# Kernel optimization log

Hardware: AMD Instinct MI355X
Metric: run time of the kernel (lower is better)

Reference implementation:

```python
import jax, jax.numpy as jnp
import numpy as np

N, E, D, H = 100000, 800000, 64, 8
DV = D // H  # v_layer output dim


def setup_inputs() -> dict:
    key = jax.random.key(0)
    ks = jax.random.split(key, 16)
    s = lambda fan_in: 1.0 / np.sqrt(fan_in)
    return {
        "atom_feat": jax.random.normal(ks[0], (N, D), jnp.float32),
        "bond_feat": jax.random.normal(ks[1], (E, D), jnp.float32),
        "edge_idx": jax.random.randint(ks[2], (E, 2), 0, N, jnp.int32),
        # v_layer: input_dim -> input_dim // att_heads
        "Wv": jax.random.normal(ks[3], (D, DV), jnp.float32) * s(D),
        "bv": jnp.zeros((DV,), jnp.float32),
        # final_att: Linear(3D, D) -> ReLU -> Linear(D, D) -> ReLU -> Linear(D, H)
        "W1": jax.random.normal(ks[4], (3 * D, D), jnp.float32) * s(3 * D),
        "b1": jnp.zeros((D,), jnp.float32),
        "W2": jax.random.normal(ks[5], (D, D), jnp.float32) * s(D),
        "b2": jnp.zeros((D,), jnp.float32),
        "W3": jax.random.normal(ks[6], (D, H), jnp.float32) * s(D),
        "b3": jnp.zeros((H,), jnp.float32),
        # conv_layer: D -> D
        "Wc": jax.random.normal(ks[7], (D, D), jnp.float32) * s(D),
        "bc": jnp.zeros((D,), jnp.float32),
        # bond_layer: 2D -> D
        "Wb": jax.random.normal(ks[8], (2 * D, D), jnp.float32) * s(2 * D),
        "bb": jnp.zeros((D,), jnp.float32),
    }


def reference(atom_feat, bond_feat, edge_idx, Wv, bv, W1, b1, W2, b2, W3, b3, Wc, bc, Wb, bb):
    n = atom_feat.shape[0]
    src, dst = edge_idx[:, 0], edge_idx[:, 1]

    # edge attention MLP: [E, 3D] -> [E, H]
    x_att = jnp.concatenate([atom_feat[dst], atom_feat[src], bond_feat], axis=-1)
    h = jax.nn.relu(x_att @ W1 + b1)
    h = jax.nn.relu(h @ W2 + b2)
    logits = h @ W3 + b3  # [E, H]

    # scatter-softmax over edges grouped by src
    seg_max = jax.ops.segment_max(logits, src, num_segments=n)
    e = jnp.exp(logits - seg_max[src])
    denom = jax.ops.segment_sum(e, src, num_segments=n)
    att = e / denom[src]  # [E, H]

    # attention-weighted scatter-sum of values
    v = atom_feat @ Wv + bv  # [N, DV]
    msg = att[:, None, :] * v[dst][:, :, None]  # [E, DV, H]
    agg = jax.ops.segment_sum(msg, src, num_segments=n)  # [N, DV, H]

    out = agg.reshape(n, -1) @ Wc + bc  # [N, D]

    # bond update
    nb = jnp.concatenate([out[dst] + out[src], bond_feat], axis=-1)  # [E, 2D]
    new_bond_feat = jax.nn.relu(nb @ Wb + bb)

    # residual + activation
    out = jax.nn.relu(atom_feat + out)
    return out, new_bond_feat
```

## Files before the change

### kernel.cpp

```cpp
#include <hip/hip_runtime.h>
#include <math.h>

#define NA 100000
#define NE 800000

typedef __attribute__((ext_vector_type(8))) short short8;
typedef __attribute__((ext_vector_type(4))) float f32x4;

__device__ __forceinline__ unsigned fmap(float f) {
    unsigned b = __float_as_uint(f);
    return (b & 0x80000000u) ? ~b : (b | 0x80000000u);
}
__device__ __forceinline__ float funmap(unsigned u) {
    unsigned b = (u & 0x80000000u) ? (u ^ 0x80000000u) : ~u;
    return __uint_as_float(b);
}
__device__ __forceinline__ unsigned short f2bf(float f) {
    unsigned u = __float_as_uint(f);
    u += 0x7fffu + ((u >> 16) & 1u);
    return (unsigned short)(u >> 16);
}

__device__ __forceinline__ short8 ldsfrag(const unsigned short* p) {
    return *(const short8*)p;
}

__global__ void k_v(const float* __restrict__ af, const float* __restrict__ Wv,
                    const float* __restrict__ bv, float* __restrict__ v) {
    __shared__ float sWv[512];
    __shared__ float sbv[8];
    int t = threadIdx.x;
    for (int i = t; i < 512; i += 256) sWv[i] = Wv[i];
    if (t < 8) sbv[t] = bv[t];
    __syncthreads();
    int gid = blockIdx.x * 256 + t;
    if (gid >= NA * 8) return;
    int n = gid >> 3, i = gid & 7;
    const float* ar = af + (long)n * 64;
    float acc = sbv[i];
#pragma unroll
    for (int k = 0; k < 64; k++) acc += ar[k] * sWv[k * 8 + i];
    v[gid] = acc;
}

__global__ __launch_bounds__(256) void k_edge_mlp(
    const float* __restrict__ af, const float* __restrict__ bond,
    const int* __restrict__ eidx,
    const float* __restrict__ W1, const float* __restrict__ b1,
    const float* __restrict__ W2, const float* __restrict__ b2,
    const float* __restrict__ W3, const float* __restrict__ b3,
    float* __restrict__ logits, unsigned* __restrict__ segmax) {
    __shared__ unsigned short sW1T[4][24][16][8];
    __shared__ unsigned short sW2T[4][8][16][8];
    __shared__ unsigned short sW3T[8][16][8];
    __shared__ unsigned short sX[4][24][16][8];
    __shared__ int sED[4][16][2];

    int tid = threadIdx.x;
    for (int idx = tid; idx < 192 * 64; idx += 256) {
        int k = idx >> 6, n = idx & 63;
        sW1T[n >> 4][k >> 3][n & 15][k & 7] = f2bf(W1[idx]);
    }
    for (int idx = tid; idx < 64 * 64; idx += 256) {
        int k = idx >> 6, n = idx & 63;
        sW2T[n >> 4][k >> 3][n & 15][k & 7] = f2bf(W2[idx]);
    }
    for (int idx = tid; idx < 8 * 16 * 8; idx += 256) ((unsigned short*)sW3T)[idx] = 0;
    __syncthreads();
    for (int idx = tid; idx < 64 * 8; idx += 256) {
        int k = idx >> 3, o = idx & 7;
        sW3T[k >> 3][o][k & 7] = f2bf(W3[idx]);
    }
    __syncthreads();

    int lane = tid & 63, wv = tid >> 6;
    int l15 = lane & 15, lq = lane >> 4;
    float b1v[4], b2v[4];
#pragma unroll
    for (int t = 0; t < 4; t++) { b1v[t] = b1[t * 16 + l15]; b2v[t] = b2[t * 16 + l15]; }
    float b3v = (l15 < 8) ? b3[l15] : 0.f;

    long stride = (long)gridDim.x * 64;
    for (long base = ((long)blockIdx.x * 4 + wv) * 16; base < NE; base += stride) {
        if (lane < 16) {
            int2 sd = ((const int2*)eidx)[base + lane];
            sED[wv][lane][0] = sd.x;
            sED[wv][lane][1] = sd.y;
        }
#pragma unroll
        for (int it = 0; it < 12; it++) {
            int q = it * 64 + lane;
            int e = q / 48;
            int r = q - e * 48;
            const float* sp;
            if (r < 16)      sp = af + (long)sED[wv][e][1] * 64 + r * 4;
            else if (r < 32) sp = af + (long)sED[wv][e][0] * 64 + (r - 16) * 4;
            else             sp = bond + (base + e) * 64 + (long)(r - 32) * 4;
            float4 xv = *(const float4*)sp;
            ushort4 p;
            p.x = f2bf(xv.x); p.y = f2bf(xv.y); p.z = f2bf(xv.z); p.w = f2bf(xv.w);
            *(ushort4*)&sX[wv][r >> 1][e][(r & 1) * 4] = p;
        }

        f32x4 acc[4] = {{0,0,0,0},{0,0,0,0},{0,0,0,0},{0,0,0,0}};
#pragma unroll
        for (int ks = 0; ks < 6; ks++) {
            short8 a = ldsfrag(&sX[wv][ks * 4 + lq][l15][0]);
#pragma unroll
            for (int t = 0; t < 4; t++) {
                short8 b = ldsfrag(&sW1T[t][ks * 4 + lq][l15][0]);
                acc[t] = __builtin_amdgcn_mfma_f32_16x16x32_bf16(a, b, acc[t], 0, 0, 0);
            }
        }
#pragma unroll
        for (int t = 0; t < 4; t++)
#pragma unroll
            for (int r = 0; r < 4; r++) {
                float h = fmaxf(acc[t][r] + b1v[t], 0.f);
                sX[wv][2 * t + ((lane >> 3) & 1)][lq * 4 + r][lane & 7] = f2bf(h);
            }

        f32x4 acc2[4] = {{0,0,0,0},{0,0,0,0},{0,0,0,0},{0,0,0,0}};
#pragma unroll
        for (int ks = 0; ks < 2; ks++) {
            short8 a = ldsfrag(&sX[wv][ks * 4 + lq][l15][0]);
#pragma unroll
            for (int t = 0; t < 4; t++) {
                short8 b = ldsfrag(&sW2T[t][ks * 4 + lq][l15][0]);
                acc2[t] = __builtin_amdgcn_mfma_f32_16x16x32_bf16(a, b, acc2[t], 0, 0, 0);
            }
        }
#pragma unroll
        for (int t = 0; t < 4; t++)
#pragma unroll
            for (int r = 0; r < 4; r++) {
                float h = fmaxf(acc2[t][r] + b2v[t], 0.f);
                sX[wv][2 * t + ((lane >> 3) & 1)][lq * 4 + r][lane & 7] = f2bf(h);
            }

        f32x4 accL = {0, 0, 0, 0};
#pragma unroll
        for (int ks = 0; ks < 2; ks++) {
            short8 a = ldsfrag(&sX[wv][ks * 4 + lq][l15][0]);
            short8 b = ldsfrag(&sW3T[ks * 4 + lq][l15][0]);
            accL = __builtin_amdgcn_mfma_f32_16x16x32_bf16(a, b, accL, 0, 0, 0);
        }
        if (l15 < 8) {
#pragma unroll
            for (int r = 0; r < 4; r++) {
                int m = lq * 4 + r;
                float lg = accL[r] + b3v;
                long e = base + m;
                logits[e * 8 + l15] = lg;
                atomicMax(&segmax[(long)sED[wv][m][0] * 8 + l15], fmap(lg));
            }
        }
    }
}

__global__ void k_exp_denom(const int* __restrict__ eidx,
                            const float* __restrict__ logits,
                            const unsigned* __restrict__ segmax,
                            float* __restrict__ denom) {
    long gid = (long)blockIdx.x * 256 + threadIdx.x;
    if (gid >= (long)NE * 8) return;
    long e = gid >> 3;
    int o = gid & 7;
    int src = eidx[2 * e];
    float m = funmap(segmax[(long)src * 8 + o]);
    float ex = __expf(logits[gid] - m);
    atomicAdd(&denom[(long)src * 8 + o], ex);
}

__global__ void k_agg(const int* __restrict__ eidx,
                      const float* __restrict__ logits,
                      const unsigned* __restrict__ segmax,
                      const float* __restrict__ denom,
                      const float* __restrict__ v,
                      float* __restrict__ agg) {
    int t = threadIdx.x;
    int lane = t & 63, wv = t >> 6;
    long e = (long)blockIdx.x * 4 + wv;
    if (e >= NE) return;
    int2 sd = ((const int2*)eidx)[e];
    int src = sd.x, dst = sd.y;
    int o = lane & 7;
    int i = lane >> 3;
    float lg = logits[e * 8 + o];
    float m = funmap(segmax[(long)src * 8 + o]);
    float den = denom[(long)src * 8 + o];
    float att = __expf(lg - m) / den;
    float val = att * v[(long)dst * 8 + i];
    atomicAdd(&agg[(long)src * 64 + lane], val);
}

__global__ __launch_bounds__(256) void k_out(
    const float* __restrict__ agg, const float* __restrict__ Wc,
    const float* __restrict__ bc, const float* __restrict__ af,
    float* __restrict__ out_pre, float* __restrict__ out_final) {
    __shared__ float sWc[64 * 64];
    int t = threadIdx.x;
    for (int i = t; i < 4096; i += 256) sWc[i] = Wc[i];
    __syncthreads();
    int lane = t & 63, wv = t >> 6;
    float bcv = bc[lane];
    long stride = (long)gridDim.x * 4;
    for (long n = (long)blockIdx.x * 4 + wv; n < NA; n += stride) {
        float a = agg[n * 64 + lane];
        float acc = bcv;
#pragma unroll 4
        for (int k = 0; k < 64; k++) acc += __shfl(a, k) * sWc[k * 64 + lane];
        out_pre[n * 64 + lane] = acc;
        out_final[n * 64 + lane] = fmaxf(af[n * 64 + lane] + acc, 0.f);
    }
}

__global__ __launch_bounds__(256) void k_bond_out(
    const float* __restrict__ out_pre, const float* __restrict__ bond,
    const int* __restrict__ eidx, const float* __restrict__ Wb,
    const float* __restrict__ bb, float* __restrict__ nbf) {
    __shared__ unsigned short sWbT[4][16][16][8];
    __shared__ unsigned short sXB[4][16][16][8];
    __shared__ int sEDB[4][16][2];

    int tid = threadIdx.x;
    for (int idx = tid; idx < 128 * 64; idx += 256) {
        int k = idx >> 6, n = idx & 63;
        sWbT[n >> 4][k >> 3][n & 15][k & 7] = f2bf(Wb[idx]);
    }
    __syncthreads();

    int lane = tid & 63, wv = tid >> 6;
    int l15 = lane & 15, lq = lane >> 4;
    float bbv[4];
#pragma unroll
    for (int t = 0; t < 4; t++) bbv[t] = bb[t * 16 + l15];

    long stride = (long)gridDim.x * 64;
    for (long base = ((long)blockIdx.x * 4 + wv) * 16; base < NE; base += stride) {
        if (lane < 16) {
            int2 sd = ((const int2*)eidx)[base + lane];
            sEDB[wv][lane][0] = sd.x;
            sEDB[wv][lane][1] = sd.y;
        }
#pragma unroll
        for (int it = 0; it < 8; it++) {
            int q = it * 64 + lane;
            int e = q >> 5;
            int r = q & 31;
            float4 xv;
            if (r < 16) {
                const float4* pa = (const float4*)(out_pre + (long)sEDB[wv][e][1] * 64 + r * 4);
                const float4* pb = (const float4*)(out_pre + (long)sEDB[wv][e][0] * 64 + r * 4);
                float4 a = *pa, b = *pb;
                xv.x = a.x + b.x; xv.y = a.y + b.y; xv.z = a.z + b.z; xv.w = a.w + b.w;
            } else {
                xv = *(const float4*)(bond + (base + e) * 64 + (long)(r - 16) * 4);
            }
            ushort4 p;
            p.x = f2bf(xv.x); p.y = f2bf(xv.y); p.z = f2bf(xv.z); p.w = f2bf(xv.w);
            *(ushort4*)&sXB[wv][r >> 1][e][(r & 1) * 4] = p;
        }

        f32x4 acc[4] = {{0,0,0,0},{0,0,0,0},{0,0,0,0},{0,0,0,0}};
#pragma unroll
        for (int ks = 0; ks < 4; ks++) {
            short8 a = ldsfrag(&sXB[wv][ks * 4 + lq][l15][0]);
#pragma unroll
            for (int t = 0; t < 4; t++) {
                short8 b = ldsfrag(&sWbT[t][ks * 4 + lq][l15][0]);
                acc[t] = __builtin_amdgcn_mfma_f32_16x16x32_bf16(a, b, acc[t], 0, 0, 0);
            }
        }
#pragma unroll
        for (int t = 0; t < 4; t++)
#pragma unroll
            for (int r = 0; r < 4; r++) {
                long m = base + lq * 4 + r;
                nbf[m * 64 + t * 16 + l15] = fmaxf(acc[t][r] + bbv[t], 0.f);
            }
    }
}

extern "C" void kernel_launch(void* const* d_in, const int* in_sizes, int n_in,
                              void* d_out, int out_size, void* d_ws, size_t ws_size,
                              hipStream_t stream) {
    const float* af   = (const float*)d_in[0];
    const float* bond = (const float*)d_in[1];
    const int*   eidx = (const int*)d_in[2];
    const float* Wv = (const float*)d_in[3];
    const float* bv = (const float*)d_in[4];
    const float* W1 = (const float*)d_in[5];
    const float* b1 = (const float*)d_in[6];
    const float* W2 = (const float*)d_in[7];
    const float* b2 = (const float*)d_in[8];
    const float* W3 = (const float*)d_in[9];
    const float* b3 = (const float*)d_in[10];
    const float* Wc = (const float*)d_in[11];
    const float* bc = (const float*)d_in[12];
    const float* Wb = (const float*)d_in[13];
    const float* bb = (const float*)d_in[14];

    float* out_final = (float*)d_out;
    float* nbf       = (float*)d_out + (long)NA * 64;

    float* ws = (float*)d_ws;
    float*    v       = ws;
    unsigned* segmax  = (unsigned*)(ws + 800000);
    float*    denom   = ws + 1600000;
    float*    logits  = ws + 2400000;
    float*    agg     = ws + 8800000;
    float*    out_pre = ws + 15200000;

    hipMemsetAsync((void*)segmax, 0, (size_t)1600000 * 4, stream);
    hipMemsetAsync((void*)agg, 0, (size_t)6400000 * 4, stream);

    k_v<<<(NA * 8 + 255) / 256, 256, 0, stream>>>(af, Wv, bv, v);

    k_edge_mlp<<<512, 256, 0, stream>>>(af, bond, eidx, W1, b1, W2, b2, W3, b3,
                                        logits, segmax);

    k_exp_denom<<<((long)NE * 8 + 255) / 256, 256, 0, stream>>>(eidx, logits,
                                                                segmax, denom);

    k_agg<<<NE / 4, 256, 0, stream>>>(eidx, logits, segmax, denom, v, agg);

    k_out<<<512, 256, 0, stream>>>(agg, Wc, bc, af, out_pre, out_final);

    k_bond_out<<<1024, 256, 0, stream>>>(out_pre, bond, eidx, Wb, bb, nbf);
}
```

Before: 1.047 ms.

## Feed MFMA from registers, fold softmax denominator into aggregation and output kernels

The edge-MLP and bond-update kernels now load gathered rows straight into bf16 MFMA fragments in registers. They compute the transposed product and pass hidden activations between layers with cross-lane shuffles instead of staging through shared memory. Weight tiles in LDS get an XOR swizzle, and launch bounds and grid sizes are raised. The separate exp/denominator kernel is removed: the aggregation kernel accumulates both the unnormalized weighted messages and the denominators, and the output kernel divides by the denominator before the Wc projection. This saves one full pass over the logits and LDS round-trips, at the cost of more register pressure and shuffle traffic.

```diff
diff --git a/kernel.cpp b/kernel.cpp
--- a/kernel.cpp
+++ b/kernel.cpp
@@ -20,9 +20,41 @@
     u += 0x7fffu + ((u >> 16) & 1u);
     return (unsigned short)(u >> 16);
 }
-
+__device__ __forceinline__ unsigned pkbf(float lo, float hi) {
+    return (unsigned)f2bf(lo) | ((unsigned)f2bf(hi) << 16);
+}
+union FragU { unsigned u[4]; short8 s; };
+__device__ __forceinline__ short8 pack_frag(float4 a, float4 b) {
+    FragU r;
+    r.u[0] = pkbf(a.x, a.y);
+    r.u[1] = pkbf(a.z, a.w);
+    r.u[2] = pkbf(b.x, b.y);
+    r.u[3] = pkbf(b.z, b.w);
+    return r.s;
+}
 __device__ __forceinline__ short8 ldsfrag(const unsigned short* p) {
     return *(const short8*)p;
+}
+__device__ __forceinline__ float4 add4(float4 a, float4 b) {
+    return make_float4(a.x + b.x, a.y + b.y, a.z + b.z, a.w + b.w);
+}
+
+__device__ __forceinline__ void trans4(const unsigned (&P)[4][2], int lq, int l15,
+                                       short8& a0, short8& a1) {
+    FragU r0, r1;
+    int up = (lq >> 1) & 1;
+#pragma unroll
+    for (int jj = 0; jj < 4; jj++) {
+        int srcl = l15 + ((2 * (lq & 1) + (jj >> 1)) << 4);
+        unsigned q0 = __shfl(P[0][jj & 1], srcl);
+        unsigned q1 = __shfl(P[1][jj & 1], srcl);
+        unsigned q2 = __shfl(P[2][jj & 1], srcl);
+        unsigned q3 = __shfl(P[3][jj & 1], srcl);
+        r0.u[jj] = up ? q1 : q0;
+        r1.u[jj] = up ? q3 : q2;
+    }
+    a0 = r0.s;
+    a1 = r1.s;
 }
 
 __global__ void k_v(const float* __restrict__ af, const float* __restrict__ Wv,
@@ -43,160 +75,155 @@
     v[gid] = acc;
 }
 
-__global__ __launch_bounds__(256) void k_edge_mlp(
+__global__ __launch_bounds__(256, 4) void k_edge_mlp(
     const float* __restrict__ af, const float* __restrict__ bond,
     const int* __restrict__ eidx,
     const float* __restrict__ W1, const float* __restrict__ b1,
     const float* __restrict__ W2, const float* __restrict__ b2,
     const float* __restrict__ W3, const float* __restrict__ b3,
     float* __restrict__ logits, unsigned* __restrict__ segmax) {
-    __shared__ unsigned short sW1T[4][24][16][8];
-    __shared__ unsigned short sW2T[4][8][16][8];
-    __shared__ unsigned short sW3T[8][16][8];
-    __shared__ unsigned short sX[4][24][16][8];
-    __shared__ int sED[4][16][2];
+    __shared__ __align__(16) unsigned short sW1T[4][24][16][8];
+    __shared__ __align__(16) unsigned short sW2T[4][8][16][8];
+    __shared__ __align__(16) unsigned short sW3T[8][16][8];
+    __shared__ __align__(16) float sb1[64], sb2[64], sb3[8];
 
     int tid = threadIdx.x;
     for (int idx = tid; idx < 192 * 64; idx += 256) {
-        int k = idx >> 6, n = idx & 63;
-        sW1T[n >> 4][k >> 3][n & 15][k & 7] = f2bf(W1[idx]);
+        int k = idx >> 6, n = idx & 63, kc = k >> 3;
+        sW1T[n >> 4][kc][(n & 15) ^ ((kc & 3) << 1)][k & 7] = f2bf(W1[idx]);
     }
     for (int idx = tid; idx < 64 * 64; idx += 256) {
-        int k = idx >> 6, n = idx & 63;
-        sW2T[n >> 4][k >> 3][n & 15][k & 7] = f2bf(W2[idx]);
+        int k = idx >> 6, n = idx & 63, kc = k >> 3;
+        sW2T[n >> 4][kc][(n & 15) ^ ((kc & 3) << 1)][k & 7] = f2bf(W2[idx]);
     }
     for (int idx = tid; idx < 8 * 16 * 8; idx += 256) ((unsigned short*)sW3T)[idx] = 0;
+    if (tid < 64) { sb1[tid] = b1[tid]; sb2[tid] = b2[tid]; }
+    if (tid < 8) sb3[tid] = b3[tid];
     __syncthreads();
     for (int idx = tid; idx < 64 * 8; idx += 256) {
-        int k = idx >> 3, o = idx & 7;
-        sW3T[k >> 3][o][k & 7] = f2bf(W3[idx]);
+        int k = idx >> 3, o = idx & 7, kc = k >> 3;
+        sW3T[kc][o ^ ((kc & 3) << 1)][k & 7] = f2bf(W3[idx]);
     }
     __syncthreads();
 
     int lane = tid & 63, wv = tid >> 6;
     int l15 = lane & 15, lq = lane >> 4;
-    float b1v[4], b2v[4];
-#pragma unroll
-    for (int t = 0; t < 4; t++) { b1v[t] = b1[t * 16 + l15]; b2v[t] = b2[t * 16 + l15]; }
-    float b3v = (l15 < 8) ? b3[l15] : 0.f;
-
-    long stride = (long)gridDim.x * 64;
-    for (long base = ((long)blockIdx.x * 4 + wv) * 16; base < NE; base += stride) {
-        if (lane < 16) {
-            int2 sd = ((const int2*)eidx)[base + lane];
-            sED[wv][lane][0] = sd.x;
-            sED[wv][lane][1] = sd.y;
-        }
-#pragma unroll
-        for (int it = 0; it < 12; it++) {
-            int q = it * 64 + lane;
-            int e = q / 48;
-            int r = q - e * 48;
-            const float* sp;
-            if (r < 16)      sp = af + (long)sED[wv][e][1] * 64 + r * 4;
-            else if (r < 32) sp = af + (long)sED[wv][e][0] * 64 + (r - 16) * 4;
-            else             sp = bond + (base + e) * 64 + (long)(r - 32) * 4;
-            float4 xv = *(const float4*)sp;
-            ushort4 p;
-            p.x = f2bf(xv.x); p.y = f2bf(xv.y); p.z = f2bf(xv.z); p.w = f2bf(xv.w);
-            *(ushort4*)&sX[wv][r >> 1][e][(r & 1) * 4] = p;
-        }
+    int swz = l15 ^ (lq << 1);
+
+    long stride = (long)gridDim.x * 4;
+    for (long tile = (long)blockIdx.x * 4 + wv; tile < NE / 16; tile += stride) {
+        long base = tile * 16;
+        long e = base + l15;
+        int2 sd = ((const int2*)eidx)[e];
+        const float* pd = af + (long)sd.y * 64 + lq * 8;
+        const float* ps = af + (long)sd.x * 64 + lq * 8;
+        const float* pb = bond + e * 64 + lq * 8;
+        float4 xv0  = *(const float4*)(pd);
+        float4 xv1  = *(const float4*)(pd + 4);
+        float4 xv2  = *(const float4*)(pd + 32);
+        float4 xv3  = *(const float4*)(pd + 36);
+        float4 xv4  = *(const float4*)(ps);
+        float4 xv5  = *(const float4*)(ps + 4);
+        float4 xv6  = *(const float4*)(ps + 32);
+        float4 xv7  = *(const float4*)(ps + 36);
+        float4 xv8  = *(const float4*)(pb);
+        float4 xv9  = *(const float4*)(pb + 4);
+        float4 xv10 = *(const float4*)(pb + 32);
+        float4 xv11 = *(const float4*)(pb + 36);
+        short8 xf0 = pack_frag(xv0, xv1);
+        short8 xf1 = pack_frag(xv2, xv3);
+        short8 xf2 = pack_frag(xv4, xv5);
+        short8 xf3 = pack_frag(xv6, xv7);
+        short8 xf4 = pack_frag(xv8, xv9);
+        short8 xf5 = pack_frag(xv10, xv11);
 
         f32x4 acc[4] = {{0,0,0,0},{0,0,0,0},{0,0,0,0},{0,0,0,0}};
 #pragma unroll
-        for (int ks = 0; ks < 6; ks++) {
-            short8 a = ldsfrag(&sX[wv][ks * 4 + lq][l15][0]);
-#pragma unroll
-            for (int t = 0; t < 4; t++) {
-                short8 b = ldsfrag(&sW1T[t][ks * 4 + lq][l15][0]);
-                acc[t] = __builtin_amdgcn_mfma_f32_16x16x32_bf16(a, b, acc[t], 0, 0, 0);
-            }
-        }
-#pragma unroll
-        for (int t = 0; t < 4; t++)
-#pragma unroll
-            for (int r = 0; r < 4; r++) {
-                float h = fmaxf(acc[t][r] + b1v[t], 0.f);
-                sX[wv][2 * t + ((lane >> 3) & 1)][lq * 4 + r][lane & 7] = f2bf(h);
-            }
-
-        f32x4 acc2[4] = {{0,0,0,0},{0,0,0,0},{0,0,0,0},{0,0,0,0}};
-#pragma unroll
-        for (int ks = 0; ks < 2; ks++) {
-            short8 a = ldsfrag(&sX[wv][ks * 4 + lq][l15][0]);
-#pragma unroll
-            for (int t = 0; t < 4; t++) {
-                short8 b = ldsfrag(&sW2T[t][ks * 4 + lq][l15][0]);
-                acc2[t] = __builtin_amdgcn_mfma_f32_16x16x32_bf16(a, b, acc2[t], 0, 0, 0);
-            }
-        }
-#pragma unroll
-        for (int t = 0; t < 4; t++)
-#pragma unroll
-            for (int r = 0; r < 4; r++) {
-                float h = fmaxf(acc2[t][r] + b2v[t], 0.f);
-                sX[wv][2 * t + ((lane >> 3) & 1)][lq * 4 + r][lane & 7] = f2bf(h);
-            }
-
-        f32x4 accL = {0, 0, 0, 0};
-#pragma unroll
-        for (int ks = 0; ks < 2; ks++) {
-            short8 a = ldsfrag(&sX[wv][ks * 4 + lq][l15][0]);
-            short8 b = ldsfrag(&sW3T[ks * 4 + lq][l15][0]);
-            accL = __builtin_amdgcn_mfma_f32_16x16x32_bf16(a, b, accL, 0, 0, 0);
-        }
-        if (l15 < 8) {
-#pragma unroll
-            for (int r = 0; r < 4; r++) {
-                int m = lq * 4 + r;
-                float lg = accL[r] + b3v;
-                long e = base + m;
-                logits[e * 8 + l15] = lg;
-                atomicMax(&segmax[(long)sED[wv][m][0] * 8 + l15], fmap(lg));
-            }
-        }
-    }
-}
-
-__global__ void k_exp_denom(const int* __restrict__ eidx,
-                            const float* __restrict__ logits,
-                            const unsigned* __restrict__ segmax,
-                            float* __restrict__ denom) {
-    long gid = (long)blockIdx.x * 256 + threadIdx.x;
-    if (gid >= (long)NE * 8) return;
-    long e = gid >> 3;
-    int o = gid & 7;
-    int src = eidx[2 * e];
-    float m = funmap(segmax[(long)src * 8 + o]);
-    float ex = __expf(logits[gid] - m);
-    atomicAdd(&denom[(long)src * 8 + o], ex);
+        for (int t = 0; t < 4; t++) {
+            acc[t] = __builtin_amdgcn_mfma_f32_16x16x32_bf16(ldsfrag(&sW1T[t][lq][swz][0]),      xf0, acc[t], 0, 0, 0);
+            acc[t] = __builtin_amdgcn_mfma_f32_16x16x32_bf16(ldsfrag(&sW1T[t][4 + lq][swz][0]),  xf1, acc[t], 0, 0, 0);
+            acc[t] = __builtin_amdgcn_mfma_f32_16x16x32_bf16(ldsfrag(&sW1T[t][8 + lq][swz][0]),  xf2, acc[t], 0, 0, 0);
+            acc[t] = __builtin_amdgcn_mfma_f32_16x16x32_bf16(ldsfrag(&sW1T[t][12 + lq][swz][0]), xf3, acc[t], 0, 0, 0);
+            acc[t] = __builtin_amdgcn_mfma_f32_16x16x32_bf16(ldsfrag(&sW1T[t][16 + lq][swz][0]), xf4, acc[t], 0, 0, 0);
+            acc[t] = __builtin_amdgcn_mfma_f32_16x16x32_bf16(ldsfrag(&sW1T[t][20 + lq][swz][0]), xf5, acc[t], 0, 0, 0);
+        }
+        unsigned P[4][2];
+#pragma unroll
+        for (int t = 0; t < 4; t++) {
+            float4 bb = *(const float4*)&sb1[t * 16 + lq * 4];
+            float h0 = fmaxf(acc[t][0] + bb.x, 0.f);
+            float h1v = fmaxf(acc[t][1] + bb.y, 0.f);
+            float h2v = fmaxf(acc[t][2] + bb.z, 0.f);
+            float h3v = fmaxf(acc[t][3] + bb.w, 0.f);
+            P[t][0] = pkbf(h0, h1v);
+            P[t][1] = pkbf(h2v, h3v);
+        }
+        short8 a0, a1;
+        trans4(P, lq, l15, a0, a1);
+
+        f32x4 ac2[4] = {{0,0,0,0},{0,0,0,0},{0,0,0,0},{0,0,0,0}};
+#pragma unroll
+        for (int t = 0; t < 4; t++) {
+            ac2[t] = __builtin_amdgcn_mfma_f32_16x16x32_bf16(ldsfrag(&sW2T[t][lq][swz][0]),     a0, ac2[t], 0, 0, 0);
+            ac2[t] = __builtin_amdgcn_mfma_f32_16x16x32_bf16(ldsfrag(&sW2T[t][4 + lq][swz][0]), a1, ac2[t], 0, 0, 0);
+        }
+#pragma unroll
+        for (int t = 0; t < 4; t++) {
+            float4 bb = *(const float4*)&sb2[t * 16 + lq * 4];
+            float h0 = fmaxf(ac2[t][0] + bb.x, 0.f);
+            float h1v = fmaxf(ac2[t][1] + bb.y, 0.f);
+            float h2v = fmaxf(ac2[t][2] + bb.z, 0.f);
+            float h3v = fmaxf(ac2[t][3] + bb.w, 0.f);
+            P[t][0] = pkbf(h0, h1v);
+            P[t][1] = pkbf(h2v, h3v);
+        }
+        trans4(P, lq, l15, a0, a1);
+
+        f32x4 aL = {0, 0, 0, 0};
+        aL = __builtin_amdgcn_mfma_f32_16x16x32_bf16(ldsfrag(&sW3T[lq][swz][0]),     a0, aL, 0, 0, 0);
+        aL = __builtin_amdgcn_mfma_f32_16x16x32_bf16(ldsfrag(&sW3T[4 + lq][swz][0]), a1, aL, 0, 0, 0);
+        if (lq < 2) {
+            float4 bb = *(const float4*)&sb3[lq * 4];
+            float4 lg;
+            lg.x = aL[0] + bb.x;
+            lg.y = aL[1] + bb.y;
+            lg.z = aL[2] + bb.z;
+            lg.w = aL[3] + bb.w;
+            *(float4*)(logits + e * 8 + lq * 4) = lg;
+            unsigned* sm = segmax + (long)sd.x * 8 + lq * 4;
+            atomicMax(sm + 0, fmap(lg.x));
+            atomicMax(sm + 1, fmap(lg.y));
+            atomicMax(sm + 2, fmap(lg.z));
+            atomicMax(sm + 3, fmap(lg.w));
+        }
+    }
 }
 
 __global__ void k_agg(const int* __restrict__ eidx,
                       const float* __restrict__ logits,
                       const unsigned* __restrict__ segmax,
-                      const float* __restrict__ denom,
                       const float* __restrict__ v,
+                      float* __restrict__ denom,
                       float* __restrict__ agg) {
     int t = threadIdx.x;
     int lane = t & 63, wv = t >> 6;
     long e = (long)blockIdx.x * 4 + wv;
     if (e >= NE) return;
     int2 sd = ((const int2*)eidx)[e];
-    int src = sd.x, dst = sd.y;
     int o = lane & 7;
     int i = lane >> 3;
     float lg = logits[e * 8 + o];
-    float m = funmap(segmax[(long)src * 8 + o]);
-    float den = denom[(long)src * 8 + o];
-    float att = __expf(lg - m) / den;
-    float val = att * v[(long)dst * 8 + i];
-    atomicAdd(&agg[(long)src * 64 + lane], val);
+    float m = funmap(segmax[(long)sd.x * 8 + o]);
+    float ex = __expf(lg - m);
+    if (i == 0) atomicAdd(&denom[(long)sd.x * 8 + o], ex);
+    float val = ex * v[(long)sd.y * 8 + i];
+    atomicAdd(&agg[(long)sd.x * 64 + lane], val);
 }
 
 __global__ __launch_bounds__(256) void k_out(
-    const float* __restrict__ agg, const float* __restrict__ Wc,
-    const float* __restrict__ bc, const float* __restrict__ af,
+    const float* __restrict__ agg, const float* __restrict__ denom,
+    const float* __restrict__ Wc, const float* __restrict__ bc,
+    const float* __restrict__ af,
     float* __restrict__ out_pre, float* __restrict__ out_final) {
     __shared__ float sWc[64 * 64];
     int t = threadIdx.x;
@@ -206,7 +233,9 @@
     float bcv = bc[lane];
     long stride = (long)gridDim.x * 4;
     for (long n = (long)blockIdx.x * 4 + wv; n < NA; n += stride) {
-        float a = agg[n * 64 + lane];
+        float den = denom[n * 8 + (lane & 7)];
+        float rs = (den != 0.f) ? (1.0f / den) : 0.f;
+        float a = agg[n * 64 + lane] * rs;
         float acc = bcv;
 #pragma unroll 4
         for (int k = 0; k < 64; k++) acc += __shfl(a, k) * sWc[k * 64 + lane];
@@ -215,70 +244,63 @@
     }
 }
 
-__global__ __launch_bounds__(256) void k_bond_out(
+__global__ __launch_bounds__(256, 4) void k_bond_out(
     const float* __restrict__ out_pre, const float* __restrict__ bond,
     const int* __restrict__ eidx, const float* __restrict__ Wb,
     const float* __restrict__ bb, float* __restrict__ nbf) {
-    __shared__ unsigned short sWbT[4][16][16][8];
-    __shared__ unsigned short sXB[4][16][16][8];
-    __shared__ int sEDB[4][16][2];
+    __shared__ __align__(16) unsigned short sWbT[4][16][16][8];
+    __shared__ __align__(16) float sbb[64];
 
     int tid = threadIdx.x;
     for (int idx = tid; idx < 128 * 64; idx += 256) {
-        int k = idx >> 6, n = idx & 63;
-        sWbT[n >> 4][k >> 3][n & 15][k & 7] = f2bf(Wb[idx]);
-    }
+        int k = idx >> 6, n = idx & 63, kc = k >> 3;
+        sWbT[n >> 4][kc][(n & 15) ^ ((kc & 3) << 1)][k & 7] = f2bf(Wb[idx]);
+    }
+    if (tid < 64) sbb[tid] = bb[tid];
     __syncthreads();
 
     int lane = tid & 63, wv = tid >> 6;
     int l15 = lane & 15, lq = lane >> 4;
-    float bbv[4];
-#pragma unroll
-    for (int t = 0; t < 4; t++) bbv[t] = bb[t * 16 + l15];
-
-    long stride = (long)gridDim.x * 64;
-    for (long base = ((long)blockIdx.x * 4 + wv) * 16; base < NE; base += stride) {
-        if (lane < 16) {
-            int2 sd = ((const int2*)eidx)[base + lane];
-            sEDB[wv][lane][0] = sd.x;
-            sEDB[wv][lane][1] = sd.y;
-        }
-#pragma unroll
-        for (int it = 0; it < 8; it++) {
-            int q = it * 64 + lane;
-            int e = q >> 5;
-            int r = q & 31;
-            float4 xv;
-            if (r < 16) {
-                const float4* pa = (const float4*)(out_pre + (long)sEDB[wv][e][1] * 64 + r * 4);
-                const float4* pb = (const float4*)(out_pre + (long)sEDB[wv][e][0] * 64 + r * 4);
-                float4 a = *pa, b = *pb;
-                xv.x = a.x + b.x; xv.y = a.y + b.y; xv.z = a.z + b.z; xv.w = a.w + b.w;
-            } else {
-                xv = *(const float4*)(bond + (base + e) * 64 + (long)(r - 16) * 4);
-            }
-            ushort4 p;
-            p.x = f2bf(xv.x); p.y = f2bf(xv.y); p.z = f2bf(xv.z); p.w = f2bf(xv.w);
-            *(ushort4*)&sXB[wv][r >> 1][e][(r & 1) * 4] = p;
-        }
+    int swz = l15 ^ (lq << 1);
+
+    long stride = (long)gridDim.x * 4;
+    for (long tile = (long)blockIdx.x * 4 + wv; tile < NE / 16; tile += stride) {
+        long base = tile * 16;
+        long e = base + l15;
+        int2 sd = ((const int2*)eidx)[e];
+        const float* pd = out_pre + (long)sd.y * 64 + lq * 8;
+        const float* ps = out_pre + (long)sd.x * 64 + lq * 8;
+        const float* pb = bond + e * 64 + lq * 8;
+        float4 d0 = *(const float4*)pd,        d1 = *(const float4*)(pd + 4);
+        float4 d2 = *(const float4*)(pd + 32), d3 = *(const float4*)(pd + 36);
+        float4 s0 = *(const float4*)ps,        s1 = *(const float4*)(ps + 4);
+        float4 s2 = *(const float4*)(ps + 32), s3 = *(const float4*)(ps + 36);
+        float4 c0 = *(const float4*)pb,        c1 = *(const float4*)(pb + 4);
+        float4 c2 = *(const float4*)(pb + 32), c3 = *(const float4*)(pb + 36);
+        short8 xf0 = pack_frag(add4(d0, s0), add4(d1, s1));
+        short8 xf1 = pack_frag(add4(d2, s2), add4(d3, s3));
+        short8 xf2 = pack_frag(c0, c1);
+        short8 xf3 = pack_frag(c2, c3);
 
         f32x4 acc[4] = {{0,0,0,0},{0,0,0,0},{0,0,0,0},{0,0,0,0}};
 #pragma unroll
-        for (int ks = 0; ks < 4; ks++) {
-            short8 a = ldsfrag(&sXB[wv][ks * 4 + lq][l15][0]);
-#pragma unroll
-            for (int t = 0; t < 4; t++) {
-                short8 b = ldsfrag(&sWbT[t][ks * 4 + lq][l15][0]);
-                acc[t] = __builtin_amdgcn_mfma_f32_16x16x32_bf16(a, b, acc[t], 0, 0, 0);
-            }
-        }
-#pragma unroll
-        for (int t = 0; t < 4; t++)
-#pragma unroll
-            for (int r = 0; r < 4; r++) {
-                long m = base + lq * 4 + r;
-                nbf[m * 64 + t * 16 + l15] = fmaxf(acc[t][r] + bbv[t], 0.f);
-            }
+        for (int t = 0; t < 4; t++) {
+            acc[t] = __builtin_amdgcn_mfma_f32_16x16x32_bf16(ldsfrag(&sWbT[t][lq][swz][0]),      xf0, acc[t], 0, 0, 0);
+            acc[t] = __builtin_amdgcn_mfma_f32_16x16x32_bf16(ldsfrag(&sWbT[t][4 + lq][swz][0]),  xf1, acc[t], 0, 0, 0);
+            acc[t] = __builtin_amdgcn_mfma_f32_16x16x32_bf16(ldsfrag(&sWbT[t][8 + lq][swz][0]),  xf2, acc[t], 0, 0, 0);
+            acc[t] = __builtin_amdgcn_mfma_f32_16x16x32_bf16(ldsfrag(&sWbT[t][12 + lq][swz][0]), xf3, acc[t], 0, 0, 0);
+        }
+        float* op = nbf + e * 64 + lq * 4;
+#pragma unroll
+        for (int t = 0; t < 4; t++) {
+            float4 bq = *(const float4*)&sbb[t * 16 + lq * 4];
+            float4 r;
+            r.x = fmaxf(acc[t][0] + bq.x, 0.f);
+            r.y = fmaxf(acc[t][1] + bq.y, 0.f);
+            r.z = fmaxf(acc[t][2] + bq.z, 0.f);
+            r.w = fmaxf(acc[t][3] + bq.w, 0.f);
+            *(float4*)(op + t * 16) = r;
+        }
     }
 }
 
@@ -317,15 +339,12 @@
 
     k_v<<<(NA * 8 + 255) / 256, 256, 0, stream>>>(af, Wv, bv, v);
 
-    k_edge_mlp<<<512, 256, 0, stream>>>(af, bond, eidx, W1, b1, W2, b2, W3, b3,
-                                        logits, segmax);
-
-    k_exp_denom<<<((long)NE * 8 + 255) / 256, 256, 0, stream>>>(eidx, logits,
-                                                                segmax, denom);
-
-    k_agg<<<NE / 4, 256, 0, stream>>>(eidx, logits, segmax, denom, v, agg);
-
-    k_out<<<512, 256, 0, stream>>>(agg, Wc, bc, af, out_pre, out_final);
-
-    k_bond_out<<<1024, 256, 0, stream>>>(out_pre, bond, eidx, Wb, bb, nbf);
-}
+    k_edge_mlp<<<1024, 256, 0, stream>>>(af, bond, eidx, W1, b1, W2, b2, W3, b3,
+                                         logits, segmax);
+
+    k_agg<<<NE / 4, 256, 0, stream>>>(eidx, logits, segmax, v, denom, agg);
+
+    k_out<<<512, 256, 0, stream>>>(agg, denom, Wc, bc, af, out_pre, out_final);
+
+    k_bond_out<<<2048, 256, 0, stream>>>(out_pre, bond, eidx, Wb, bb, nbf);
+}
```

After: 1.129 ms. 7.8% more time.
